# Kernel optimization log

Hardware: AMD Instinct MI355X
Metric: run time of the kernel (lower is better)

## Reference

```python
import jax, jax.numpy as jnp
import numpy as np

B, S, E, H = 4, 2048, 1024, 16
D = E // H
MAX_DIST = 4
LN_EPS = 1e-5


def setup_inputs() -> dict:
    key = jax.random.key(0)
    ks = jax.random.split(key, 12)
    std = 1.0 / np.sqrt(E)
    inp = {
        "x": jax.random.normal(ks[0], (B, S, E), dtype=jnp.float32),
        "distances": jax.random.randint(ks[1], (B, S, S), 0, 5, dtype=jnp.int64),
        "Wq": jax.random.normal(ks[2], (E, E), dtype=jnp.float32) * std,
        "bq": jnp.zeros((E,), dtype=jnp.float32),
        "Wk": jax.random.normal(ks[3], (E, E), dtype=jnp.float32) * std,
        "bk": jnp.zeros((E,), dtype=jnp.float32),
        "Wv": jax.random.normal(ks[4], (E, E), dtype=jnp.float32) * std,
        "bv": jnp.zeros((E,), dtype=jnp.float32),
        "Wo": jax.random.normal(ks[5], (E, E), dtype=jnp.float32) * std,
        "bo": jnp.zeros((E,), dtype=jnp.float32),
        "dist_bias": jax.random.normal(ks[6], (MAX_DIST + 1,), dtype=jnp.float32) * 0.1,
        "ln_g": jnp.ones((E,), dtype=jnp.float32),
        "ln_b": jnp.zeros((E,), dtype=jnp.float32),
    }
    return inp


def _layernorm(y, g, b):
    mu = jnp.mean(y, axis=-1, keepdims=True)
    var = jnp.mean(jnp.square(y - mu), axis=-1, keepdims=True)
    return (y - mu) * jax.lax.rsqrt(var + LN_EPS) * g + b


def reference(x, distances, Wq, bq, Wk, bk, Wv, bv, Wo, bo, dist_bias, ln_g, ln_b):
    scale = 1.0 / np.sqrt(D)
    # projections (torch Linear: x @ W.T + b), split into heads -> [B,H,S,D]
    def heads(y):
        return y.reshape(B, S, H, D).transpose(0, 2, 1, 3)
    q = heads(x @ Wq.T + bq)
    k = heads(x @ Wk.T + bk)
    v = heads(x @ Wv.T + bv)
    scores = jnp.einsum('bhsd,bhtd->bhst', q, k) * scale  # [B,H,S,S]
    d = jnp.clip(distances, 0, MAX_DIST)
    bias = dist_bias[d]  # [B,S,S] gather from learned table
    scores = scores + bias[:, None, :, :]
    attn = jax.nn.softmax(scores, axis=-1)
    out = jnp.einsum('bhst,bhtd->bhsd', attn, v)
    out = out.transpose(0, 2, 1, 3).reshape(B, S, E)
    out = out @ Wo.T + bo
    return _layernorm(x + out, ln_g, ln_b)
```

## Files before the change

### kernel.cpp

```cpp
#include <hip/hip_runtime.h>
#include <stdint.h>

#define NB 4
#define NS 2048
#define NE 1024
#define NH 16
#define ND 64
#define LN_EPS 1e-5f

typedef __attribute__((ext_vector_type(8))) unsigned short u16x8;
typedef __attribute__((ext_vector_type(4))) unsigned short u16x4;
typedef __attribute__((ext_vector_type(8))) short b16x8;
typedef __attribute__((ext_vector_type(4))) float f32x4;

static __device__ __forceinline__ unsigned short f2bf(float f) {
  unsigned u = __builtin_bit_cast(unsigned, f);
  u += 0x7FFFu + ((u >> 16) & 1u);
  return (unsigned short)(u >> 16);
}
static __device__ __forceinline__ float bf2f(unsigned short h) {
  return __builtin_bit_cast(float, (unsigned)h << 16);
}
static __device__ __forceinline__ float bperm_f(int addr, float v) {
  return __builtin_bit_cast(float,
      __builtin_amdgcn_ds_bpermute(addr, __builtin_bit_cast(int, v)));
}
static __device__ __forceinline__ unsigned cvtpk(float lo, float hi) {
  unsigned r;
  asm("v_cvt_pk_bf16_f32 %0, %1, %2" : "=v"(r) : "v"(lo), "v"(hi));
  return r;
}

#define MFMA16(a, b, c) __builtin_amdgcn_mfma_f32_16x16x32_bf16( \
    __builtin_bit_cast(b16x8, a), __builtin_bit_cast(b16x8, b), c, 0, 0, 0)

__global__ void k_cvt(const float* __restrict__ src, unsigned short* __restrict__ dst, int n) {
  int i = (blockIdx.x * 256 + threadIdx.x) * 8;
  if (i >= n) return;
  float4 a = *(const float4*)(src + i);
  float4 b = *(const float4*)(src + i + 4);
  u16x8 o;
  o[0]=f2bf(a.x); o[1]=f2bf(a.y); o[2]=f2bf(a.z); o[3]=f2bf(a.w);
  o[4]=f2bf(b.x); o[5]=f2bf(b.y); o[6]=f2bf(b.z); o[7]=f2bf(b.w);
  *(u16x8*)(dst + i) = o;
}

__global__ void k_bias(const int* __restrict__ d, const float* __restrict__ tbl,
                       unsigned short* __restrict__ bias) {
  size_t i = ((size_t)blockIdx.x * 256 + threadIdx.x) * 8;
  int4 a = *(const int4*)(d + i);
  int4 b = *(const int4*)(d + i + 4);
  u16x8 o;
  int v;
  v = a.x; v = v < 0 ? 0 : (v > 4 ? 4 : v); o[0] = f2bf(tbl[v]);
  v = a.y; v = v < 0 ? 0 : (v > 4 ? 4 : v); o[1] = f2bf(tbl[v]);
  v = a.z; v = v < 0 ? 0 : (v > 4 ? 4 : v); o[2] = f2bf(tbl[v]);
  v = a.w; v = v < 0 ? 0 : (v > 4 ? 4 : v); o[3] = f2bf(tbl[v]);
  v = b.x; v = v < 0 ? 0 : (v > 4 ? 4 : v); o[4] = f2bf(tbl[v]);
  v = b.y; v = v < 0 ? 0 : (v > 4 ? 4 : v); o[5] = f2bf(tbl[v]);
  v = b.z; v = v < 0 ? 0 : (v > 4 ? 4 : v); o[6] = f2bf(tbl[v]);
  v = b.w; v = v < 0 ? 0 : (v > 4 ? 4 : v); o[7] = f2bf(tbl[v]);
  *(u16x8*)(bias + i) = o;
}

__global__ __launch_bounds__(256, 2) void k_qkv(
    const unsigned short* __restrict__ xb,
    const unsigned short* __restrict__ wq, const unsigned short* __restrict__ wk_,
    const unsigned short* __restrict__ wv,
    const float* __restrict__ bq, const float* __restrict__ bk_, const float* __restrict__ bv,
    unsigned short* __restrict__ q, unsigned short* __restrict__ kk,
    unsigned short* __restrict__ vt) {
  __shared__ unsigned short sA[128 * 40];
  __shared__ unsigned short sB[128 * 40];
  const int tid = threadIdx.x;
  const int lane = tid & 63, wid = tid >> 6;
  const int g = lane >> 4, c16 = lane & 15;
  const int wm = wid >> 1, wn = wid & 1;
  const int z = blockIdx.z;
  const unsigned short* w = (z == 0) ? wq : ((z == 1) ? wk_ : wv);
  const float* bias = (z == 0) ? bq : ((z == 1) ? bk_ : bv);
  const int n0 = blockIdx.x * 128, m0 = blockIdx.y * 128;

  f32x4 acc[4][4];
#pragma unroll
  for (int i = 0; i < 4; ++i)
#pragma unroll
    for (int j = 0; j < 4; ++j) acc[i][j] = f32x4{0.f, 0.f, 0.f, 0.f};

  const int srow = tid >> 2, scol = (tid & 3) * 8;

  for (int k0 = 0; k0 < NE; k0 += 32) {
#pragma unroll
    for (int i = 0; i < 2; ++i) {
      int row = srow + i * 64;
      u16x8 av = *(const u16x8*)(xb + (size_t)(m0 + row) * NE + k0 + scol);
      u16x8 bw = *(const u16x8*)(w + (size_t)(n0 + row) * NE + k0 + scol);
      *(u16x8*)(sA + row * 40 + scol) = av;
      *(u16x8*)(sB + row * 40 + scol) = bw;
    }
    __syncthreads();
    u16x8 af[4], bfr[4];
#pragma unroll
    for (int mt = 0; mt < 4; ++mt)
      af[mt] = *(const u16x8*)(sA + (wm * 64 + mt * 16 + c16) * 40 + g * 8);
#pragma unroll
    for (int nt = 0; nt < 4; ++nt)
      bfr[nt] = *(const u16x8*)(sB + (wn * 64 + nt * 16 + c16) * 40 + g * 8);
#pragma unroll
    for (int mt = 0; mt < 4; ++mt)
#pragma unroll
      for (int nt = 0; nt < 4; ++nt)
        acc[mt][nt] = MFMA16(af[mt], bfr[nt], acc[mt][nt]);
    __syncthreads();
  }

  if (z < 2) {
    unsigned short* dst = (z == 0) ? q : kk;
#pragma unroll
    for (int mt = 0; mt < 4; ++mt)
#pragma unroll
      for (int nt = 0; nt < 4; ++nt) {
        int col = n0 + wn * 64 + nt * 16 + c16;
        float bb = bias[col];
#pragma unroll
        for (int rr = 0; rr < 4; ++rr) {
          int row = m0 + wm * 64 + mt * 16 + g * 4 + rr;
          dst[(size_t)row * NE + col] = f2bf(acc[mt][nt][rr] + bb);
        }
      }
  } else {
#pragma unroll
    for (int mt = 0; mt < 4; ++mt)
#pragma unroll
      for (int nt = 0; nt < 4; ++nt) {
        int col = n0 + wn * 64 + nt * 16 + c16;
        float bb = bias[col];
        int h = col >> 6, dd = col & 63;
        int grow = m0 + wm * 64 + mt * 16 + g * 4;
        int b = grow >> 11, ss = grow & 2047;
        u16x4 o;
#pragma unroll
        for (int rr = 0; rr < 4; ++rr) o[rr] = f2bf(acc[mt][nt][rr] + bb);
        *(u16x4*)(vt + ((size_t)((b * NH + h) * ND + dd)) * NS + ss) = o;
      }
  }
}

__global__ __launch_bounds__(256, 2) void k_attn(
    const unsigned short* __restrict__ q, const unsigned short* __restrict__ kk,
    const unsigned short* __restrict__ vt, const unsigned short* __restrict__ bias,
    unsigned short* __restrict__ attn) {
  __shared__ unsigned short sK[64 * 72];
  __shared__ unsigned short sV[64 * 72];
  __shared__ unsigned short sP[4][16 * 72];
  const int tid = threadIdx.x, lane = tid & 63, wid = tid >> 6;
  const int g = lane >> 4, c16 = lane & 15;
  const int flat = blockIdx.x;
  const int kdec = flat >> 3;
  const int h = kdec & 15;
  const int G = (flat & 7) | ((kdec >> 4) << 3);
  const int b = G >> 4, qb = G & 15;
  const int q0 = qb * 128 + wid * 32;
  const size_t qkbase = ((size_t)b * NS) * NE + (size_t)h * ND;
  const size_t vbase = ((size_t)(b * NH + h) * ND) * NS;
  const size_t bbase = (size_t)b * NS * NS;
  unsigned short* sPw = &sP[wid][0];

  u16x8 qf[2][2];
#pragma unroll
  for (int mt = 0; mt < 2; ++mt)
#pragma unroll
    for (int dc = 0; dc < 2; ++dc)
      qf[mt][dc] = *(const u16x8*)(q + qkbase + (size_t)(q0 + mt * 16 + c16) * NE + dc * 32 + g * 8);

  f32x4 oa[2][4];
  float m[2], l[2];
#pragma unroll
  for (int mt = 0; mt < 2; ++mt) {
#pragma unroll
    for (int dt = 0; dt < 4; ++dt) oa[mt][dt] = f32x4{0.f, 0.f, 0.f, 0.f};
    m[mt] = -1e30f; l[mt] = 0.f;
  }

  int addr_rr[4];
#pragma unroll
  for (int rr = 0; rr < 4; ++rr) addr_rr[rr] = (g * 20 + rr) * 4;

  const int srow = tid >> 3, scol = (tid & 7) * 8;
  u16x8 rk0, rk1, rv0, rv1;
  u16x4 bp[2][4];

  auto issue_kv = [&](int kt) {
    rk0 = *(const u16x8*)(kk + qkbase + (size_t)(kt + srow) * NE + scol);
    rk1 = *(const u16x8*)(kk + qkbase + (size_t)(kt + srow + 32) * NE + scol);
    rv0 = *(const u16x8*)(vt + vbase + (size_t)srow * NS + kt + scol);
    rv1 = *(const u16x8*)(vt + vbase + (size_t)(srow + 32) * NS + kt + scol);
  };
  auto issue_bias = [&](int kt) {
#pragma unroll
    for (int mt = 0; mt < 2; ++mt)
#pragma unroll
      for (int nt = 0; nt < 4; ++nt)
        bp[mt][nt] = *(const u16x4*)(bias + bbase +
            (size_t)(q0 + mt * 16 + c16) * NS + kt + nt * 16 + g * 4);
  };

  issue_kv(0);
  issue_bias(0);

  for (int kt = 0; kt < NS; kt += 64) {
    __syncthreads();
    *(u16x8*)(sK + srow * 72 + scol) = rk0;
    *(u16x8*)(sK + (srow + 32) * 72 + scol) = rk1;
    *(u16x8*)(sV + srow * 72 + scol) = rv0;
    *(u16x8*)(sV + (srow + 32) * 72 + scol) = rv1;
    __syncthreads();
    if (kt + 64 < NS) issue_kv(kt + 64);

    f32x4 p[2][4];
#pragma unroll
    for (int nt = 0; nt < 4; ++nt) {
      u16x8 kf0 = *(const u16x8*)(sK + (nt * 16 + c16) * 72 + g * 8);
      u16x8 kf1 = *(const u16x8*)(sK + (nt * 16 + c16) * 72 + 32 + g * 8);
#pragma unroll
      for (int mt = 0; mt < 2; ++mt) {
        f32x4 t = f32x4{0.f, 0.f, 0.f, 0.f};
        t = MFMA16(kf0, qf[mt][0], t);
        t = MFMA16(kf1, qf[mt][1], t);
        p[mt][nt] = t;
      }
    }

#pragma unroll
    for (int mt = 0; mt < 2; ++mt) {
      float v[4][4];
#pragma unroll
      for (int nt = 0; nt < 4; ++nt)
#pragma unroll
        for (int rr = 0; rr < 4; ++rr)
          v[nt][rr] = p[mt][nt][rr] * 0.125f + bf2f(bp[mt][nt][rr]);
      float mx = v[0][0];
#pragma unroll
      for (int nt = 0; nt < 4; ++nt)
#pragma unroll
        for (int rr = 0; rr < 4; ++rr) mx = fmaxf(mx, v[nt][rr]);
      mx = fmaxf(mx, __shfl_xor(mx, 16));
      mx = fmaxf(mx, __shfl_xor(mx, 32));
      if (__any(mx > m[mt] + 4.0f)) {
        float nm = fmaxf(m[mt], mx);
        float al = __expf(m[mt] - nm);
        m[mt] = nm;
        l[mt] *= al;
#pragma unroll
        for (int rr = 0; rr < 4; ++rr) {
          float alr = bperm_f(addr_rr[rr], al);
#pragma unroll
          for (int dt = 0; dt < 4; ++dt) oa[mt][dt][rr] *= alr;
        }
      }
      float rs = 0.f;
#pragma unroll
      for (int nt = 0; nt < 4; ++nt)
#pragma unroll
        for (int rr = 0; rr < 4; ++rr) {
          float e = __expf(v[nt][rr] - m[mt]);
          v[nt][rr] = e;
          rs += e;
        }
      rs += __shfl_xor(rs, 16);
      rs += __shfl_xor(rs, 32);
      l[mt] += rs;
#pragma unroll
      for (int nt = 0; nt < 4; ++nt) {
        unsigned w0 = cvtpk(v[nt][0], v[nt][1]);
        unsigned w1 = cvtpk(v[nt][2], v[nt][3]);
        *(unsigned long long*)(sPw + c16 * 72 + nt * 16 + g * 4) =
            ((unsigned long long)w1 << 32) | (unsigned long long)w0;
      }
      if (mt == 1 && kt + 64 < NS) issue_bias(kt + 64);
#pragma unroll
      for (int h2 = 0; h2 < 2; ++h2) {
        u16x8 pa = *(const u16x8*)(sPw + c16 * 72 + h2 * 32 + g * 8);
#pragma unroll
        for (int dt = 0; dt < 4; ++dt) {
          u16x8 vb = *(const u16x8*)(sV + (dt * 16 + c16) * 72 + h2 * 32 + g * 8);
          oa[mt][dt] = MFMA16(pa, vb, oa[mt][dt]);
        }
      }
    }
  }

#pragma unroll
  for (int mt = 0; mt < 2; ++mt) {
    float invl = 1.0f / l[mt];
    float invr[4];
#pragma unroll
    for (int rr = 0; rr < 4; ++rr) invr[rr] = bperm_f(addr_rr[rr], invl);
#pragma unroll
    for (int dt = 0; dt < 4; ++dt)
#pragma unroll
      for (int rr = 0; rr < 4; ++rr) {
        int row = q0 + mt * 16 + g * 4 + rr;
        attn[qkbase + (size_t)row * NE + dt * 16 + c16] = f2bf(oa[mt][dt][rr] * invr[rr]);
      }
  }
}

__global__ __launch_bounds__(256, 2) void k_proj(
    const unsigned short* __restrict__ a, const unsigned short* __restrict__ w,
    const float* __restrict__ bo, const float* __restrict__ x, float* __restrict__ y) {
  __shared__ unsigned short sA[128 * 40];
  __shared__ unsigned short sB[128 * 40];
  const int tid = threadIdx.x;
  const int lane = tid & 63, wid = tid >> 6;
  const int g = lane >> 4, c16 = lane & 15;
  const int wm = wid >> 1, wn = wid & 1;
  const int n0 = blockIdx.x * 128, m0 = blockIdx.y * 128;

  f32x4 acc[4][4];
#pragma unroll
  for (int i = 0; i < 4; ++i)
#pragma unroll
    for (int j = 0; j < 4; ++j) acc[i][j] = f32x4{0.f, 0.f, 0.f, 0.f};

  const int srow = tid >> 2, scol = (tid & 3) * 8;

  for (int k0 = 0; k0 < NE; k0 += 32) {
#pragma unroll
    for (int i = 0; i < 2; ++i) {
      int row = srow + i * 64;
      u16x8 av = *(const u16x8*)(a + (size_t)(m0 + row) * NE + k0 + scol);
      u16x8 bw = *(const u16x8*)(w + (size_t)(n0 + row) * NE + k0 + scol);
      *(u16x8*)(sA + row * 40 + scol) = av;
      *(u16x8*)(sB + row * 40 + scol) = bw;
    }
    __syncthreads();
    u16x8 af[4], bfr[4];
#pragma unroll
    for (int mt = 0; mt < 4; ++mt)
      af[mt] = *(const u16x8*)(sA + (wm * 64 + mt * 16 + c16) * 40 + g * 8);
#pragma unroll
    for (int nt = 0; nt < 4; ++nt)
      bfr[nt] = *(const u16x8*)(sB + (wn * 64 + nt * 16 + c16) * 40 + g * 8);
#pragma unroll
    for (int mt = 0; mt < 4; ++mt)
#pragma unroll
      for (int nt = 0; nt < 4; ++nt)
        acc[mt][nt] = MFMA16(af[mt], bfr[nt], acc[mt][nt]);
    __syncthreads();
  }

#pragma unroll
  for (int mt = 0; mt < 4; ++mt)
#pragma unroll
    for (int nt = 0; nt < 4; ++nt) {
      int col = n0 + wn * 64 + nt * 16 + c16;
      float bb = bo[col];
#pragma unroll
      for (int rr = 0; rr < 4; ++rr) {
        int row = m0 + wm * 64 + mt * 16 + g * 4 + rr;
        y[(size_t)row * NE + col] = acc[mt][nt][rr] + bb + x[(size_t)row * NE + col];
      }
    }
}

__global__ void k_ln(const float* __restrict__ y, const float* __restrict__ gg,
                     const float* __restrict__ bb, float* __restrict__ out) {
  const int row = blockIdx.x, tid = threadIdx.x;
  float4 v = *(const float4*)(y + (size_t)row * NE + tid * 4);
  float s = v.x + v.y + v.z + v.w;
  float s2 = v.x * v.x + v.y * v.y + v.z * v.z + v.w * v.w;
#pragma unroll
  for (int off = 1; off < 64; off <<= 1) {
    s += __shfl_xor(s, off);
    s2 += __shfl_xor(s2, off);
  }
  __shared__ float red[8];
  const int wid = tid >> 6, lane = tid & 63;
  if (lane == 0) { red[wid * 2] = s; red[wid * 2 + 1] = s2; }
  __syncthreads();
  s = red[0] + red[2] + red[4] + red[6];
  s2 = red[1] + red[3] + red[5] + red[7];
  float mu = s * (1.0f / NE);
  float var = s2 * (1.0f / NE) - mu * mu;
  float rstd = rsqrtf(var + LN_EPS);
  float4 g4 = *(const float4*)(gg + tid * 4);
  float4 b4 = *(const float4*)(bb + tid * 4);
  float4 o;
  o.x = (v.x - mu) * rstd * g4.x + b4.x;
  o.y = (v.y - mu) * rstd * g4.y + b4.y;
  o.z = (v.z - mu) * rstd * g4.z + b4.z;
  o.w = (v.w - mu) * rstd * g4.w + b4.w;
  *(float4*)(out + (size_t)row * NE + tid * 4) = o;
}

extern "C" void kernel_launch(void* const* d_in, const int* in_sizes, int n_in,
                              void* d_out, int out_size, void* d_ws, size_t ws_size,
                              hipStream_t stream) {
  (void)in_sizes; (void)n_in; (void)out_size; (void)ws_size;
  const float* x = (const float*)d_in[0];
  const int* dist = (const int*)d_in[1];
  const float* Wq = (const float*)d_in[2];
  const float* bq = (const float*)d_in[3];
  const float* Wk = (const float*)d_in[4];
  const float* bk = (const float*)d_in[5];
  const float* Wv = (const float*)d_in[6];
  const float* bv = (const float*)d_in[7];
  const float* Wo = (const float*)d_in[8];
  const float* bo = (const float*)d_in[9];
  const float* tbl = (const float*)d_in[10];
  const float* lng = (const float*)d_in[11];
  const float* lnb = (const float*)d_in[12];
  float* out = (float*)d_out;

  char* ws = (char*)d_ws;
  size_t off = 0;
  auto alloc = [&](size_t bytes) {
    char* p = ws + off;
    off += (bytes + 255) & ~(size_t)255;
    return p;
  };
  unsigned short* xb = (unsigned short*)d_out;
  unsigned short* wqb = (unsigned short*)alloc((size_t)NE * NE * 2);
  unsigned short* wkb = (unsigned short*)alloc((size_t)NE * NE * 2);
  unsigned short* wvb = (unsigned short*)alloc((size_t)NE * NE * 2);
  unsigned short* wob = (unsigned short*)alloc((size_t)NE * NE * 2);
  unsigned short* qq  = (unsigned short*)alloc((size_t)NB * NS * NE * 2);
  unsigned short* kb  = (unsigned short*)alloc((size_t)NB * NS * NE * 2);
  unsigned short* vtb = (unsigned short*)alloc((size_t)NB * NS * NE * 2);
  unsigned short* attn = (unsigned short*)alloc((size_t)NB * NS * NE * 2);
  unsigned short* bias = (unsigned short*)alloc((size_t)NB * NS * NS * 2);
  float* y = out;

  k_cvt<<<NB * NS * NE / 2048, 256, 0, stream>>>(x, xb, NB * NS * NE);
  k_cvt<<<NE * NE / 2048, 256, 0, stream>>>(Wq, wqb, NE * NE);
  k_cvt<<<NE * NE / 2048, 256, 0, stream>>>(Wk, wkb, NE * NE);
  k_cvt<<<NE * NE / 2048, 256, 0, stream>>>(Wv, wvb, NE * NE);
  k_cvt<<<NE * NE / 2048, 256, 0, stream>>>(Wo, wob, NE * NE);
  k_bias<<<(NB * NS * NS) / 2048, 256, 0, stream>>>(dist, tbl, bias);
  k_qkv<<<dim3(NE / 128, NB * NS / 128, 3), 256, 0, stream>>>(
      xb, wqb, wkb, wvb, bq, bk, bv, qq, kb, vtb);
  k_attn<<<dim3(NB * NS / 128 * NH), 256, 0, stream>>>(qq, kb, vtb, bias, attn);
  k_proj<<<dim3(NE / 128, NB * NS / 128), 256, 0, stream>>>(attn, wob, bo, x, y);
  k_ln<<<NB * NS, 256, 0, stream>>>(y, lng, lnb, out);
}
```

Before: 321.1 us.

## Double-buffer K/V in LDS with XOR swizzle and exp2-based softmax

The attention kernel now keeps two LDS buffers for K and V, so each iteration needs one barrier instead of two. The padded 72-element rows become 64-element rows with an XOR swizzle on the 16-byte slots to avoid bank conflicts. Softmax is moved to base-2: the scale and the distance-bias table are pre-multiplied by log2(e) and exp2 replaces expf. The lazy-rescale threshold is raised from 4 to 6 to match the base-2 units. The cost is a larger LDS footprint, which may limit occupancy, and a lazy-rescale headroom that changes slightly in natural-log units.

```diff
diff --git a/kernel.cpp b/kernel.cpp
--- a/kernel.cpp
+++ b/kernel.cpp
@@ -7,6 +7,7 @@
 #define NH 16
 #define ND 64
 #define LN_EPS 1e-5f
+#define LN2I 1.44269504089f
 
 typedef __attribute__((ext_vector_type(8))) unsigned short u16x8;
 typedef __attribute__((ext_vector_type(4))) unsigned short u16x4;
@@ -30,6 +31,11 @@
   asm("v_cvt_pk_bf16_f32 %0, %1, %2" : "=v"(r) : "v"(lo), "v"(hi));
   return r;
 }
+#if __has_builtin(__builtin_amdgcn_exp2f)
+static __device__ __forceinline__ float ex2(float x) { return __builtin_amdgcn_exp2f(x); }
+#else
+static __device__ __forceinline__ float ex2(float x) { return exp2f(x); }
+#endif
 
 #define MFMA16(a, b, c) __builtin_amdgcn_mfma_f32_16x16x32_bf16( \
     __builtin_bit_cast(b16x8, a), __builtin_bit_cast(b16x8, b), c, 0, 0, 0)
@@ -52,14 +58,14 @@
   int4 b = *(const int4*)(d + i + 4);
   u16x8 o;
   int v;
-  v = a.x; v = v < 0 ? 0 : (v > 4 ? 4 : v); o[0] = f2bf(tbl[v]);
-  v = a.y; v = v < 0 ? 0 : (v > 4 ? 4 : v); o[1] = f2bf(tbl[v]);
-  v = a.z; v = v < 0 ? 0 : (v > 4 ? 4 : v); o[2] = f2bf(tbl[v]);
-  v = a.w; v = v < 0 ? 0 : (v > 4 ? 4 : v); o[3] = f2bf(tbl[v]);
-  v = b.x; v = v < 0 ? 0 : (v > 4 ? 4 : v); o[4] = f2bf(tbl[v]);
-  v = b.y; v = v < 0 ? 0 : (v > 4 ? 4 : v); o[5] = f2bf(tbl[v]);
-  v = b.z; v = v < 0 ? 0 : (v > 4 ? 4 : v); o[6] = f2bf(tbl[v]);
-  v = b.w; v = v < 0 ? 0 : (v > 4 ? 4 : v); o[7] = f2bf(tbl[v]);
+  v = a.x; v = v < 0 ? 0 : (v > 4 ? 4 : v); o[0] = f2bf(tbl[v] * LN2I);
+  v = a.y; v = v < 0 ? 0 : (v > 4 ? 4 : v); o[1] = f2bf(tbl[v] * LN2I);
+  v = a.z; v = v < 0 ? 0 : (v > 4 ? 4 : v); o[2] = f2bf(tbl[v] * LN2I);
+  v = a.w; v = v < 0 ? 0 : (v > 4 ? 4 : v); o[3] = f2bf(tbl[v] * LN2I);
+  v = b.x; v = v < 0 ? 0 : (v > 4 ? 4 : v); o[4] = f2bf(tbl[v] * LN2I);
+  v = b.y; v = v < 0 ? 0 : (v > 4 ? 4 : v); o[5] = f2bf(tbl[v] * LN2I);
+  v = b.z; v = v < 0 ? 0 : (v > 4 ? 4 : v); o[6] = f2bf(tbl[v] * LN2I);
+  v = b.w; v = v < 0 ? 0 : (v > 4 ? 4 : v); o[7] = f2bf(tbl[v] * LN2I);
   *(u16x8*)(bias + i) = o;
 }
 
@@ -150,9 +156,9 @@
     const unsigned short* __restrict__ q, const unsigned short* __restrict__ kk,
     const unsigned short* __restrict__ vt, const unsigned short* __restrict__ bias,
     unsigned short* __restrict__ attn) {
-  __shared__ unsigned short sK[64 * 72];
-  __shared__ unsigned short sV[64 * 72];
-  __shared__ unsigned short sP[4][16 * 72];
+  __shared__ unsigned short sK[2][64 * 64];
+  __shared__ unsigned short sV[2][64 * 64];
+  __shared__ unsigned short sP[4][16 * 64];
   const int tid = threadIdx.x, lane = tid & 63, wid = tid >> 6;
   const int g = lane >> 4, c16 = lane & 15;
   const int flat = blockIdx.x;
@@ -186,15 +192,22 @@
 #pragma unroll
   for (int rr = 0; rr < 4; ++rr) addr_rr[rr] = (g * 20 + rr) * 4;
 
-  const int srow = tid >> 3, scol = (tid & 7) * 8;
+  const int srow = tid >> 3, sslot = tid & 7;
+  const int w_off = srow * 64 + ((sslot ^ (srow & 7)) << 3);
+  const int rs0 = (g ^ (c16 & 7)) << 3;
+  const int rs1 = ((g + 4) ^ (c16 & 7)) << 3;
+  const int pw_base = c16 * 64 + (g & 1) * 4;
+  const int pr0 = c16 * 64 + ((g ^ (c16 & 7)) << 3);
+  const int pr1 = c16 * 64 + (((4 + g) ^ (c16 & 7)) << 3);
+
   u16x8 rk0, rk1, rv0, rv1;
   u16x4 bp[2][4];
 
   auto issue_kv = [&](int kt) {
-    rk0 = *(const u16x8*)(kk + qkbase + (size_t)(kt + srow) * NE + scol);
-    rk1 = *(const u16x8*)(kk + qkbase + (size_t)(kt + srow + 32) * NE + scol);
-    rv0 = *(const u16x8*)(vt + vbase + (size_t)srow * NS + kt + scol);
-    rv1 = *(const u16x8*)(vt + vbase + (size_t)(srow + 32) * NS + kt + scol);
+    rk0 = *(const u16x8*)(kk + qkbase + (size_t)(kt + srow) * NE + sslot * 8);
+    rk1 = *(const u16x8*)(kk + qkbase + (size_t)(kt + srow + 32) * NE + sslot * 8);
+    rv0 = *(const u16x8*)(vt + vbase + (size_t)srow * NS + kt + sslot * 8);
+    rv1 = *(const u16x8*)(vt + vbase + (size_t)(srow + 32) * NS + kt + sslot * 8);
   };
   auto issue_bias = [&](int kt) {
 #pragma unroll
@@ -208,20 +221,22 @@
   issue_kv(0);
   issue_bias(0);
 
-  for (int kt = 0; kt < NS; kt += 64) {
+  for (int kt = 0, it = 0; kt < NS; kt += 64, ++it) {
+    unsigned short* bK = &sK[it & 1][0];
+    unsigned short* bV = &sV[it & 1][0];
+    *(u16x8*)(bK + w_off) = rk0;
+    *(u16x8*)(bK + w_off + 32 * 64) = rk1;
+    *(u16x8*)(bV + w_off) = rv0;
+    *(u16x8*)(bV + w_off + 32 * 64) = rv1;
+    if (kt + 64 < NS) issue_kv(kt + 64);
     __syncthreads();
-    *(u16x8*)(sK + srow * 72 + scol) = rk0;
-    *(u16x8*)(sK + (srow + 32) * 72 + scol) = rk1;
-    *(u16x8*)(sV + srow * 72 + scol) = rv0;
-    *(u16x8*)(sV + (srow + 32) * 72 + scol) = rv1;
-    __syncthreads();
-    if (kt + 64 < NS) issue_kv(kt + 64);
 
     f32x4 p[2][4];
 #pragma unroll
     for (int nt = 0; nt < 4; ++nt) {
-      u16x8 kf0 = *(const u16x8*)(sK + (nt * 16 + c16) * 72 + g * 8);
-      u16x8 kf1 = *(const u16x8*)(sK + (nt * 16 + c16) * 72 + 32 + g * 8);
+      const unsigned short* kr = bK + nt * 1024 + c16 * 64;
+      u16x8 kf0 = *(const u16x8*)(kr + rs0);
+      u16x8 kf1 = *(const u16x8*)(kr + rs1);
 #pragma unroll
       for (int mt = 0; mt < 2; ++mt) {
         f32x4 t = f32x4{0.f, 0.f, 0.f, 0.f};
@@ -238,7 +253,7 @@
       for (int nt = 0; nt < 4; ++nt)
 #pragma unroll
         for (int rr = 0; rr < 4; ++rr)
-          v[nt][rr] = p[mt][nt][rr] * 0.125f + bf2f(bp[mt][nt][rr]);
+          v[nt][rr] = p[mt][nt][rr] * (0.125f * LN2I) + bf2f(bp[mt][nt][rr]);
       float mx = v[0][0];
 #pragma unroll
       for (int nt = 0; nt < 4; ++nt)
@@ -246,9 +261,9 @@
         for (int rr = 0; rr < 4; ++rr) mx = fmaxf(mx, v[nt][rr]);
       mx = fmaxf(mx, __shfl_xor(mx, 16));
       mx = fmaxf(mx, __shfl_xor(mx, 32));
-      if (__any(mx > m[mt] + 4.0f)) {
+      if (__any(mx > m[mt] + 6.0f)) {
         float nm = fmaxf(m[mt], mx);
-        float al = __expf(m[mt] - nm);
+        float al = ex2(m[mt] - nm);
         m[mt] = nm;
         l[mt] *= al;
 #pragma unroll
@@ -263,7 +278,7 @@
       for (int nt = 0; nt < 4; ++nt)
 #pragma unroll
         for (int rr = 0; rr < 4; ++rr) {
-          float e = __expf(v[nt][rr] - m[mt]);
+          float e = ex2(v[nt][rr] - m[mt]);
           v[nt][rr] = e;
           rs += e;
         }
@@ -274,16 +289,17 @@
       for (int nt = 0; nt < 4; ++nt) {
         unsigned w0 = cvtpk(v[nt][0], v[nt][1]);
         unsigned w1 = cvtpk(v[nt][2], v[nt][3]);
-        *(unsigned long long*)(sPw + c16 * 72 + nt * 16 + g * 4) =
+        *(unsigned long long*)(sPw + pw_base +
+            (((2 * nt + (g >> 1)) ^ (c16 & 7)) << 3)) =
             ((unsigned long long)w1 << 32) | (unsigned long long)w0;
       }
       if (mt == 1 && kt + 64 < NS) issue_bias(kt + 64);
 #pragma unroll
       for (int h2 = 0; h2 < 2; ++h2) {
-        u16x8 pa = *(const u16x8*)(sPw + c16 * 72 + h2 * 32 + g * 8);
+        u16x8 pa = *(const u16x8*)(sPw + (h2 ? pr1 : pr0));
 #pragma unroll
         for (int dt = 0; dt < 4; ++dt) {
-          u16x8 vb = *(const u16x8*)(sV + (dt * 16 + c16) * 72 + h2 * 32 + g * 8);
+          u16x8 vb = *(const u16x8*)(bV + dt * 1024 + c16 * 64 + (h2 ? rs1 : rs0));
           oa[mt][dt] = MFMA16(pa, vb, oa[mt][dt]);
         }
       }
```

Result: faster. 313.3 us (-2.4%).
